# Performance work log

Hardware: AMD Instinct MI355X
Metric: run time of the kernel (lower is better)

## Reference

```python
import jax, jax.numpy as jnp
import numpy as np

N_ATOMS = 100000
N_EDGES = 1000000
HIDDEN = 64
OUT_DIM = 128
N_LAYERS = 3
N_ELEMENTS = 100


def setup_inputs() -> dict:
    key = jax.random.key(0)
    ks = jax.random.split(key, 14)
    s = 0.05
    return {
        "atomic_numbers": jax.random.randint(ks[0], (N_ATOMS,), 0, N_ELEMENTS),
        "positions": jax.random.normal(ks[1], (N_ATOMS, 3), jnp.float32),
        "lattice": jax.random.normal(ks[2], (3, 3), jnp.float32),
        "edge_index": jax.random.randint(ks[3], (2, N_EDGES), 0, N_ATOMS),
        "emb_table": jax.random.normal(ks[4], (N_ELEMENTS, HIDDEN), jnp.float32) * s,
        "W_lin": jax.random.normal(ks[5], (N_LAYERS, HIDDEN, HIDDEN), jnp.float32) * s,
        "b_lin": jax.random.normal(ks[6], (N_LAYERS, HIDDEN), jnp.float32) * s,
        "W_gate": jax.random.normal(ks[7], (N_LAYERS, 2 * HIDDEN, HIDDEN), jnp.float32) * s,
        "b_gate": jax.random.normal(ks[8], (N_LAYERS, HIDDEN), jnp.float32) * s,
        "W_out1": jax.random.normal(ks[9], (HIDDEN, HIDDEN), jnp.float32) * s,
        "b_out1": jax.random.normal(ks[10], (HIDDEN,), jnp.float32) * s,
        "W_out2": jax.random.normal(ks[11], (HIDDEN, OUT_DIM), jnp.float32) * s,
        "b_out2": jax.random.normal(ks[12], (OUT_DIM,), jnp.float32) * s,
    }


def reference(atomic_numbers, positions, lattice, edge_index,
              emb_table, W_lin, b_lin, W_gate, b_gate,
              W_out1, b_out1, W_out2, b_out2):
    # positions/lattice unused when edge_index is provided (matches original).
    x = emb_table[atomic_numbers]            # [N, H] embedding lookup
    row, col = edge_index[0], edge_index[1]
    n = x.shape[0]
    for i in range(W_lin.shape[0]):          # fixed small layer count
        xn = x[col]                          # [E, H] neighbor gather
        gate_in = jnp.concatenate([x[row], xn], axis=-1)  # [E, 2H]
        gate = jax.nn.sigmoid(gate_in @ W_gate[i] + b_gate[i])
        messages = gate * (xn @ W_lin[i] + b_lin[i])       # [E, H]
        agg = jax.ops.segment_sum(messages, row, num_segments=n)  # scatter-add
        x = jax.nn.relu(agg + x @ W_lin[i] + b_lin[i])
    pooled = x.mean(axis=0)                  # [H] mean pool over atoms
    h = jax.nn.relu(pooled @ W_out1 + b_out1)
    return h @ W_out2 + b_out2               # [OUT_DIM]
```

## Files before the change

### kernel.cpp

```cpp
#include <hip/hip_runtime.h>
#include <hip/hip_bf16.h>
#include <stdint.h>


#define H 64
#define BSHIFT 7
#define BROWS 128

typedef __attribute__((ext_vector_type(8))) short bf16x8;
typedef __attribute__((ext_vector_type(4))) float f32x4;

__device__ __forceinline__ float sigmoidf_fast(float z) {
  return __builtin_amdgcn_rcpf(1.f + __expf(-z));
}

__device__ __forceinline__ ushort f2bf(float f) {
  uint32_t u = __float_as_uint(f);
  u = (u + 0x7fffu + ((u >> 16) & 1u)) >> 16;
  return (ushort)u;
}
__device__ __forceinline__ uint32_t pack_gl(float gc, float lin) {
  uint32_t ug = __float_as_uint(gc);
  ug = (ug + 0x7fffu + ((ug >> 16) & 1u)) >> 16;
  uint32_t ul = __float_as_uint(lin);
  ul = ((ul + 0x7fffu + ((ul >> 16) & 1u)) >> 16) << 16;
  return ul | ug;
}
__device__ __forceinline__ float unpack_gc(uint32_t p) {
  return __uint_as_float(p << 16);
}
__device__ __forceinline__ float unpack_lin(uint32_t p) {
  return __uint_as_float(p & 0xffff0000u);
}

__global__ __launch_bounds__(256) void bucket_hist_kernel(
    const int* __restrict__ row, int* __restrict__ bcnt, int E, int nbuck) {
  __shared__ int cnt[1024];
  const int tid = threadIdx.x;
  for (int b = tid; b < nbuck; b += 256) cnt[b] = 0;
  __syncthreads();
  for (int e = blockIdx.x * blockDim.x + tid; e < E; e += gridDim.x * blockDim.x)
    atomicAdd(&cnt[row[e] >> BSHIFT], 1);
  __syncthreads();
  for (int b = tid; b < nbuck; b += 256)
    if (cnt[b]) atomicAdd(&bcnt[b], cnt[b]);
}

__global__ __launch_bounds__(1024) void bucket_scan_kernel(
    const int* __restrict__ bcnt, int* __restrict__ bstart,
    int* __restrict__ bcur, int* __restrict__ offs, int nbuck, int N, int E) {
  __shared__ int sh[1024];
  const int tid = threadIdx.x;
  const int mine = (tid < nbuck) ? bcnt[tid] : 0;
  sh[tid] = mine;
  __syncthreads();
  for (int off = 1; off < 1024; off <<= 1) {
    const int v = (tid >= off) ? sh[tid - off] : 0;
    __syncthreads();
    sh[tid] += v;
    __syncthreads();
  }
  if (tid < nbuck) {
    const int ex = sh[tid] - mine;
    bstart[tid] = ex;
    bcur[tid] = ex;
  }
  if (tid == 0) {
    bstart[nbuck] = E;
    offs[N] = E;
  }
}

#define SCHUNK 4096
__global__ __launch_bounds__(256) void bucket_scatter_kernel(
    const int* __restrict__ row, const int* __restrict__ col,
    int* __restrict__ bcur, uint2* __restrict__ ebuf, int E, int nbuck) {
  __shared__ int cnt[1024], base[1024];
  const int tid = threadIdx.x;
  const int start = blockIdx.x * SCHUNK;
  const int end = min(start + SCHUNK, E);
  for (int b = tid; b < nbuck; b += 256) cnt[b] = 0;
  __syncthreads();
  for (int e = start + tid; e < end; e += 256)
    atomicAdd(&cnt[row[e] >> BSHIFT], 1);
  __syncthreads();
  for (int b = tid; b < nbuck; b += 256) {
    if (cnt[b]) base[b] = atomicAdd(&bcur[b], cnt[b]);
    cnt[b] = 0;
  }
  __syncthreads();
  for (int e = start + tid; e < end; e += 256) {
    const int r = row[e];
    const int b = r >> BSHIFT;
    const int pos = base[b] + atomicAdd(&cnt[b], 1);
    ebuf[pos] = make_uint2((uint32_t)r, (uint32_t)col[e]);
  }
}

__global__ __launch_bounds__(256) void csr_build_kernel(
    const uint2* __restrict__ ebuf, const int* __restrict__ bstart,
    int* __restrict__ offs, int* __restrict__ cols, int N) {
  __shared__ int cnt[BROWS], sc[BROWS];
  const int tid = threadIdx.x;
  const int b = blockIdx.x;
  const int bs = bstart[b], be = bstart[b + 1];
  const int rowbase = b << BSHIFT;
  if (tid < BROWS) cnt[tid] = 0;
  __syncthreads();
  for (int e = bs + tid; e < be; e += 256)
    atomicAdd(&cnt[ebuf[e].x & (BROWS - 1)], 1);
  __syncthreads();
  if (tid < BROWS) sc[tid] = cnt[tid];
  __syncthreads();
  for (int off = 1; off < BROWS; off <<= 1) {
    const int v = (tid >= off && tid < BROWS) ? sc[tid - off] : 0;
    __syncthreads();
    if (tid < BROWS) sc[tid] += v;
    __syncthreads();
  }
  if (tid < BROWS) {
    sc[tid] -= cnt[tid];
    cnt[tid] = 0;
    const int r = rowbase + tid;
    if (r < N) offs[r] = bs + sc[tid];
  }
  __syncthreads();
  for (int e = bs + tid; e < be; e += 256) {
    const uint2 u = ebuf[e];
    const int rl = u.x & (BROWS - 1);
    const int pos = sc[rl] + atomicAdd(&cnt[rl], 1);
    cols[bs + pos] = (int)u.y;
  }
}

template <bool FIRST>
__global__ __launch_bounds__(256) void node_mm3_mfma(
    const ushort* __restrict__ x, const int* __restrict__ an,
    const float* __restrict__ emb, const float* __restrict__ Wl,
    const float* __restrict__ bl, const float* __restrict__ Wgr,
    const float* __restrict__ Wgc, const float* __restrict__ bg,
    float* __restrict__ gr, uint32_t* __restrict__ glpk, int N) {
  const int tid = threadIdx.x;
  const int lane = tid & 63, wid = tid >> 6;
  const int l15 = lane & 15, kg = lane >> 4;

  bf16x8 bfrag[3][4][2];
#pragma unroll
  for (int mat = 0; mat < 3; mat++) {
    const float* Wm = (mat == 0) ? Wl : (mat == 1) ? Wgr : Wgc;
#pragma unroll
    for (int nt = 0; nt < 4; nt++) {
#pragma unroll
      for (int ks = 0; ks < 2; ks++) {
        const float* wp = Wm + (size_t)(ks * 32 + kg * 8) * H + nt * 16 + l15;
        bf16x8 bb;
#pragma unroll
        for (int j = 0; j < 8; j++) bb[j] = (short)f2bf(wp[(size_t)j * H]);
        bfrag[mat][nt][ks] = bb;
      }
    }
  }

  const int mbase = blockIdx.x * 64 + wid * 16;
  const int arow = mbase + l15;
  const int arow_c = min(arow, N - 1);

  bf16x8 afrag0, afrag1;
  if (FIRST) {
    const int a = an[arow_c];
    const float* src = emb + (size_t)a * H + kg * 8;
    const float4 u0 = *(const float4*)(src);
    const float4 u1 = *(const float4*)(src + 4);
    const float4 u2 = *(const float4*)(src + 32);
    const float4 u3 = *(const float4*)(src + 36);
    bf16x8 t0, t1;
    t0[0] = (short)f2bf(u0.x); t0[1] = (short)f2bf(u0.y);
    t0[2] = (short)f2bf(u0.z); t0[3] = (short)f2bf(u0.w);
    t0[4] = (short)f2bf(u1.x); t0[5] = (short)f2bf(u1.y);
    t0[6] = (short)f2bf(u1.z); t0[7] = (short)f2bf(u1.w);
    t1[0] = (short)f2bf(u2.x); t1[1] = (short)f2bf(u2.y);
    t1[2] = (short)f2bf(u2.z); t1[3] = (short)f2bf(u2.w);
    t1[4] = (short)f2bf(u3.x); t1[5] = (short)f2bf(u3.y);
    t1[6] = (short)f2bf(u3.z); t1[7] = (short)f2bf(u3.w);
    afrag0 = t0; afrag1 = t1;
  } else {
    const ushort* src = x + (size_t)arow_c * H + kg * 8;
    afrag0 = *(const bf16x8*)(src);
    afrag1 = *(const bf16x8*)(src + 32);
  }

  f32x4 accL[4], accR[4], accC[4];
#pragma unroll
  for (int nt = 0; nt < 4; nt++) {
    const float blv = bl[nt * 16 + l15];
    const float bgv = bg[nt * 16 + l15];
    accL[nt] = (f32x4){blv, blv, blv, blv};
    accR[nt] = (f32x4){0.f, 0.f, 0.f, 0.f};
    accC[nt] = (f32x4){bgv, bgv, bgv, bgv};
  }
#pragma unroll
  for (int nt = 0; nt < 4; nt++) {
    accL[nt] = __builtin_amdgcn_mfma_f32_16x16x32_bf16(afrag0, bfrag[0][nt][0], accL[nt], 0, 0, 0);
    accL[nt] = __builtin_amdgcn_mfma_f32_16x16x32_bf16(afrag1, bfrag[0][nt][1], accL[nt], 0, 0, 0);
    accR[nt] = __builtin_amdgcn_mfma_f32_16x16x32_bf16(afrag0, bfrag[1][nt][0], accR[nt], 0, 0, 0);
    accR[nt] = __builtin_amdgcn_mfma_f32_16x16x32_bf16(afrag1, bfrag[1][nt][1], accR[nt], 0, 0, 0);
    accC[nt] = __builtin_amdgcn_mfma_f32_16x16x32_bf16(afrag0, bfrag[2][nt][0], accC[nt], 0, 0, 0);
    accC[nt] = __builtin_amdgcn_mfma_f32_16x16x32_bf16(afrag1, bfrag[2][nt][1], accC[nt], 0, 0, 0);
  }
#pragma unroll
  for (int nt = 0; nt < 4; nt++) {
#pragma unroll
    for (int r = 0; r < 4; r++) {
      const int atom = mbase + kg * 4 + r;
      if (atom < N) {
        const size_t o = (size_t)atom * H + nt * 16 + l15;
        gr[o] = accR[nt][r];
        glpk[o] = pack_gl(accC[nt][r], accL[nt][r]);
      }
    }
  }
}

__global__ __launch_bounds__(256) void agg_kernel(
    const float* __restrict__ gr, const uint32_t* __restrict__ glpk,
    const int* __restrict__ offs, const int* __restrict__ cols,
    ushort* __restrict__ x, int N) {
  const int lane = threadIdx.x & 63, w = threadIdx.x >> 6;
  for (int i = blockIdx.x * 4 + w; i < N; i += gridDim.x * 4) {
    const int s = offs[i], e = offs[i + 1];
    const float gri = gr[(size_t)i * H + lane];
    float acc = 0.f;
    for (int cb = s; cb < e; cb += 64) {
      const int nchunk = min(64, e - cb);
      const int myc = (lane < nchunk) ? cols[cb + lane] : 0;
      int j = 0;
      for (; j + 3 < nchunk; j += 4) {
        const int c0 = __shfl(myc, j + 0), c1 = __shfl(myc, j + 1);
        const int c2 = __shfl(myc, j + 2), c3 = __shfl(myc, j + 3);
        const uint32_t p0 = glpk[(size_t)c0 * H + lane];
        const uint32_t p1 = glpk[(size_t)c1 * H + lane];
        const uint32_t p2 = glpk[(size_t)c2 * H + lane];
        const uint32_t p3 = glpk[(size_t)c3 * H + lane];
        acc += unpack_lin(p0) * sigmoidf_fast(gri + unpack_gc(p0));
        acc += unpack_lin(p1) * sigmoidf_fast(gri + unpack_gc(p1));
        acc += unpack_lin(p2) * sigmoidf_fast(gri + unpack_gc(p2));
        acc += unpack_lin(p3) * sigmoidf_fast(gri + unpack_gc(p3));
      }
      for (; j < nchunk; j++) {
        const int c0 = __shfl(myc, j);
        const uint32_t p0 = glpk[(size_t)c0 * H + lane];
        acc += unpack_lin(p0) * sigmoidf_fast(gri + unpack_gc(p0));
      }
    }
    const float li = unpack_lin(glpk[(size_t)i * H + lane]);
    x[(size_t)i * H + lane] = f2bf(fmaxf(acc + li, 0.f));
  }
}

__global__ void pool_kernel(const ushort* __restrict__ x,
                            float* __restrict__ pool, int N) {
  __shared__ float ps[4][64];
  const int tid = threadIdx.x, c = tid & 63, wid = tid >> 6;
  float s = 0.f;
  for (int i = blockIdx.x * 4 + wid; i < N; i += gridDim.x * 4)
    s += __uint_as_float(((uint32_t)x[(size_t)i * H + c]) << 16);
  ps[wid][c] = s;
  __syncthreads();
  if (tid < 64) {
    const float t = ps[0][tid] + ps[1][tid] + ps[2][tid] + ps[3][tid];
    atomicAdd(&pool[tid], t);
  }
}

__global__ void mlp_kernel(const float* __restrict__ pool,
                           const float* __restrict__ W1,
                           const float* __restrict__ b1,
                           const float* __restrict__ W2,
                           const float* __restrict__ b2,
                           float* __restrict__ out, float invN) {
  __shared__ float p[64], h[64];
  const int tid = threadIdx.x;
  if (tid < 64) p[tid] = pool[tid] * invN;
  __syncthreads();
  if (tid < 64) {
    float s = b1[tid];
    for (int k = 0; k < 64; k++) s = fmaf(p[k], W1[k * 64 + tid], s);
    h[tid] = fmaxf(s, 0.f);
  }
  __syncthreads();
  float s = b2[tid];
  for (int k = 0; k < 64; k++) s = fmaf(h[k], W2[k * 128 + tid], s);
  out[tid] = s;
}

extern "C" void kernel_launch(void* const* d_in, const int* in_sizes, int n_in,
                              void* d_out, int out_size, void* d_ws,
                              size_t ws_size, hipStream_t stream) {
  const int*   an  = (const int*)d_in[0];
  const int*   ei  = (const int*)d_in[3];
  const float* emb = (const float*)d_in[4];
  const float* Wl  = (const float*)d_in[5];
  const float* bl  = (const float*)d_in[6];
  const float* Wg  = (const float*)d_in[7];
  const float* bg  = (const float*)d_in[8];
  const float* W1  = (const float*)d_in[9];
  const float* b1  = (const float*)d_in[10];
  const float* W2  = (const float*)d_in[11];
  const float* b2  = (const float*)d_in[12];
  float* out = (float*)d_out;

  const int N = in_sizes[0];
  const int E = in_sizes[3] / 2;
  const int* row = ei;
  const int* col = ei + E;
  const int nbuck = (N + BROWS - 1) >> BSHIFT;

  const size_t NH = (size_t)N * H;
  char* ws = (char*)d_ws;
  ushort*   x    = (ushort*)(ws);
  float*    gr   = (float*)(ws + NH * 2);
  uint32_t* glpk = (uint32_t*)(ws + NH * 2 + NH * 4);
  char* p = ws + NH * 2 + NH * 4 + NH * 4;
  int*   offs   = (int*)p;   p += ((size_t)N + 1) * 4;
  int*   cols   = (int*)p;   p += (size_t)E * 4;
  int*   bcnt   = (int*)p;   p += 4096;
  int*   bstart = (int*)p;   p += 4100;
  int*   bcur   = (int*)p;   p += 4096;
  uint2* ebuf   = (uint2*)p; p += (size_t)E * 8;
  float* pool   = (float*)p;

  hipMemsetAsync(bcnt, 0, (size_t)nbuck * 4, stream);
  bucket_hist_kernel<<<1024, 256, 0, stream>>>(row, bcnt, E, nbuck);
  bucket_scan_kernel<<<1, 1024, 0, stream>>>(bcnt, bstart, bcur, offs, nbuck, N, E);
  bucket_scatter_kernel<<<(E + SCHUNK - 1) / SCHUNK, 256, 0, stream>>>(
      row, col, bcur, ebuf, E, nbuck);
  csr_build_kernel<<<nbuck, 256, 0, stream>>>(ebuf, bstart, offs, cols, N);

  const int mmGrid = (N + 63) / 64;
  const int aggGrid = (N + 3) / 4;
  for (int l = 0; l < 3; l++) {
    const float* Wl_l  = Wl + (size_t)l * H * H;
    const float* bl_l  = bl + (size_t)l * H;
    const float* Wgr_l = Wg + (size_t)l * 2 * H * H;
    const float* Wgc_l = Wgr_l + H * H;
    const float* bg_l  = bg + (size_t)l * H;
    if (l == 0)
      node_mm3_mfma<true><<<mmGrid, 256, 0, stream>>>(
          x, an, emb, Wl_l, bl_l, Wgr_l, Wgc_l, bg_l, gr, glpk, N);
    else
      node_mm3_mfma<false><<<mmGrid, 256, 0, stream>>>(
          x, an, emb, Wl_l, bl_l, Wgr_l, Wgc_l, bg_l, gr, glpk, N);
    agg_kernel<<<aggGrid, 256, 0, stream>>>(gr, glpk, offs, cols, x, N);
  }

  hipMemsetAsync(pool, 0, 64 * sizeof(float), stream);
  pool_kernel<<<1024, 256, 0, stream>>>(x, pool, N);
  mlp_kernel<<<1, 128, 0, stream>>>(pool, W1, b1, W2, b2, out, 1.0f / (float)N);
}
```

Baseline: 403.7 us.

## Pre-pack bf16 weight fragments, fold -log2e into gate weights, unroll gather by 8

Adds a prep kernel that converts the layer weights once into bf16 MFMA fragment layout, with the gate weights and gate bias pre-scaled by -log2(e). This lets the aggregation compute the sigmoid with exp2 and no multiply, and removes the per-block strided fp32 loads and conversions in the node matmul. The edge-gather loop is unrolled to 8 loads in flight to expose more memory parallelism. The pool memset is folded into the scan kernel. Scaling before bf16 rounding changes rounding slightly, and the extra prep launch adds a small fixed cost.

```diff
diff --git a/kernel.cpp b/kernel.cpp
--- a/kernel.cpp
+++ b/kernel.cpp
@@ -6,13 +6,10 @@
 #define H 64
 #define BSHIFT 7
 #define BROWS 128
+#define NLOG2E -1.4426950408889634f
 
 typedef __attribute__((ext_vector_type(8))) short bf16x8;
 typedef __attribute__((ext_vector_type(4))) float f32x4;
-
-__device__ __forceinline__ float sigmoidf_fast(float z) {
-  return __builtin_amdgcn_rcpf(1.f + __expf(-z));
-}
 
 __device__ __forceinline__ ushort f2bf(float f) {
   uint32_t u = __float_as_uint(f);
@@ -32,6 +29,36 @@
 __device__ __forceinline__ float unpack_lin(uint32_t p) {
   return __uint_as_float(p & 0xffff0000u);
 }
+__device__ __forceinline__ float sig_from_neglog2(float arg) {
+  return __builtin_amdgcn_rcpf(1.f + exp2f(arg));
+}
+
+__global__ __launch_bounds__(256) void prep_kernel(
+    const float* __restrict__ Wl, const float* __restrict__ Wg,
+    const float* __restrict__ bg, bf16x8* __restrict__ wprep,
+    float* __restrict__ bgs) {
+  const int t = blockIdx.x * 256 + threadIdx.x;
+  if (t < 192) bgs[t] = bg[t] * NLOG2E;
+  if (t >= 4608) return;
+  const int l = t / 1536;
+  const int rem = t - l * 1536;
+  const int mat = rem >> 9;
+  const int rem2 = rem & 511;
+  const int nt = rem2 >> 7;
+  const int ks = (rem2 >> 6) & 1;
+  const int lane = rem2 & 63;
+  const int kg = lane >> 4, l15 = lane & 15;
+  const float* src;
+  float s;
+  if (mat == 0)      { src = Wl + (size_t)l * 4096;        s = 1.f; }
+  else if (mat == 1) { src = Wg + (size_t)l * 8192;        s = NLOG2E; }
+  else               { src = Wg + (size_t)l * 8192 + 4096; s = NLOG2E; }
+  bf16x8 v;
+#pragma unroll
+  for (int j = 0; j < 8; j++)
+    v[j] = (short)f2bf(src[(size_t)(ks * 32 + kg * 8 + j) * 64 + nt * 16 + l15] * s);
+  wprep[t] = v;
+}
 
 __global__ __launch_bounds__(256) void bucket_hist_kernel(
     const int* __restrict__ row, int* __restrict__ bcnt, int E, int nbuck) {
@@ -48,9 +75,11 @@
 
 __global__ __launch_bounds__(1024) void bucket_scan_kernel(
     const int* __restrict__ bcnt, int* __restrict__ bstart,
-    int* __restrict__ bcur, int* __restrict__ offs, int nbuck, int N, int E) {
+    int* __restrict__ bcur, int* __restrict__ offs, float* __restrict__ pool,
+    int nbuck, int N, int E) {
   __shared__ int sh[1024];
   const int tid = threadIdx.x;
+  if (tid < 64) pool[tid] = 0.f;
   const int mine = (tid < nbuck) ? bcnt[tid] : 0;
   sh[tid] = mine;
   __syncthreads();
@@ -136,9 +165,8 @@
 template <bool FIRST>
 __global__ __launch_bounds__(256) void node_mm3_mfma(
     const ushort* __restrict__ x, const int* __restrict__ an,
-    const float* __restrict__ emb, const float* __restrict__ Wl,
-    const float* __restrict__ bl, const float* __restrict__ Wgr,
-    const float* __restrict__ Wgc, const float* __restrict__ bg,
+    const float* __restrict__ emb, const bf16x8* __restrict__ wp,
+    const float* __restrict__ bl, const float* __restrict__ bgs,
     float* __restrict__ gr, uint32_t* __restrict__ glpk, int N) {
   const int tid = threadIdx.x;
   const int lane = tid & 63, wid = tid >> 6;
@@ -146,20 +174,12 @@
 
   bf16x8 bfrag[3][4][2];
 #pragma unroll
-  for (int mat = 0; mat < 3; mat++) {
-    const float* Wm = (mat == 0) ? Wl : (mat == 1) ? Wgr : Wgc;
-#pragma unroll
-    for (int nt = 0; nt < 4; nt++) {
-#pragma unroll
-      for (int ks = 0; ks < 2; ks++) {
-        const float* wp = Wm + (size_t)(ks * 32 + kg * 8) * H + nt * 16 + l15;
-        bf16x8 bb;
-#pragma unroll
-        for (int j = 0; j < 8; j++) bb[j] = (short)f2bf(wp[(size_t)j * H]);
-        bfrag[mat][nt][ks] = bb;
-      }
-    }
-  }
+  for (int mat = 0; mat < 3; mat++)
+#pragma unroll
+    for (int nt = 0; nt < 4; nt++)
+#pragma unroll
+      for (int ks = 0; ks < 2; ks++)
+        bfrag[mat][nt][ks] = wp[(((mat * 4 + nt) * 2 + ks) << 6) + lane];
 
   const int mbase = blockIdx.x * 64 + wid * 16;
   const int arow = mbase + l15;
@@ -193,7 +213,7 @@
 #pragma unroll
   for (int nt = 0; nt < 4; nt++) {
     const float blv = bl[nt * 16 + l15];
-    const float bgv = bg[nt * 16 + l15];
+    const float bgv = bgs[nt * 16 + l15];
     accL[nt] = (f32x4){blv, blv, blv, blv};
     accR[nt] = (f32x4){0.f, 0.f, 0.f, 0.f};
     accC[nt] = (f32x4){bgv, bgv, bgv, bgv};
@@ -234,22 +254,21 @@
       const int nchunk = min(64, e - cb);
       const int myc = (lane < nchunk) ? cols[cb + lane] : 0;
       int j = 0;
-      for (; j + 3 < nchunk; j += 4) {
-        const int c0 = __shfl(myc, j + 0), c1 = __shfl(myc, j + 1);
-        const int c2 = __shfl(myc, j + 2), c3 = __shfl(myc, j + 3);
-        const uint32_t p0 = glpk[(size_t)c0 * H + lane];
-        const uint32_t p1 = glpk[(size_t)c1 * H + lane];
-        const uint32_t p2 = glpk[(size_t)c2 * H + lane];
-        const uint32_t p3 = glpk[(size_t)c3 * H + lane];
-        acc += unpack_lin(p0) * sigmoidf_fast(gri + unpack_gc(p0));
-        acc += unpack_lin(p1) * sigmoidf_fast(gri + unpack_gc(p1));
-        acc += unpack_lin(p2) * sigmoidf_fast(gri + unpack_gc(p2));
-        acc += unpack_lin(p3) * sigmoidf_fast(gri + unpack_gc(p3));
+      for (; j + 7 < nchunk; j += 8) {
+        uint32_t p[8];
+#pragma unroll
+        for (int q = 0; q < 8; q++) {
+          const int c = __shfl(myc, j + q);
+          p[q] = glpk[(size_t)c * H + lane];
+        }
+#pragma unroll
+        for (int q = 0; q < 8; q++)
+          acc += unpack_lin(p[q]) * sig_from_neglog2(gri + unpack_gc(p[q]));
       }
       for (; j < nchunk; j++) {
-        const int c0 = __shfl(myc, j);
-        const uint32_t p0 = glpk[(size_t)c0 * H + lane];
-        acc += unpack_lin(p0) * sigmoidf_fast(gri + unpack_gc(p0));
+        const int c = __shfl(myc, j);
+        const uint32_t p0 = glpk[(size_t)c * H + lane];
+        acc += unpack_lin(p0) * sig_from_neglog2(gri + unpack_gc(p0));
       }
     }
     const float li = unpack_lin(glpk[(size_t)i * H + lane]);
@@ -321,17 +340,22 @@
   float*    gr   = (float*)(ws + NH * 2);
   uint32_t* glpk = (uint32_t*)(ws + NH * 2 + NH * 4);
   char* p = ws + NH * 2 + NH * 4 + NH * 4;
-  int*   offs   = (int*)p;   p += ((size_t)N + 1) * 4;
-  int*   cols   = (int*)p;   p += (size_t)E * 4;
-  int*   bcnt   = (int*)p;   p += 4096;
-  int*   bstart = (int*)p;   p += 4100;
-  int*   bcur   = (int*)p;   p += 4096;
-  uint2* ebuf   = (uint2*)p; p += (size_t)E * 8;
-  float* pool   = (float*)p;
+  int*    offs   = (int*)p;    p += ((size_t)N + 1) * 4;
+  int*    cols   = (int*)p;    p += (size_t)E * 4;
+  int*    bcnt   = (int*)p;    p += 4096;
+  int*    bstart = (int*)p;    p += 4100;
+  int*    bcur   = (int*)p;    p += 4096;
+  uint2*  ebuf   = (uint2*)p;  p += (size_t)E * 8;
+  bf16x8* wprep  = (bf16x8*)p; p += 4608 * 16;
+  float*  bgs    = (float*)p;  p += 192 * 4;
+  float*  pool   = (float*)p;
+
+  prep_kernel<<<18, 256, 0, stream>>>(Wl, Wg, bg, wprep, bgs);
 
   hipMemsetAsync(bcnt, 0, (size_t)nbuck * 4, stream);
   bucket_hist_kernel<<<1024, 256, 0, stream>>>(row, bcnt, E, nbuck);
-  bucket_scan_kernel<<<1, 1024, 0, stream>>>(bcnt, bstart, bcur, offs, nbuck, N, E);
+  bucket_scan_kernel<<<1, 1024, 0, stream>>>(bcnt, bstart, bcur, offs, pool,
+                                             nbuck, N, E);
   bucket_scatter_kernel<<<(E + SCHUNK - 1) / SCHUNK, 256, 0, stream>>>(
       row, col, bcur, ebuf, E, nbuck);
   csr_build_kernel<<<nbuck, 256, 0, stream>>>(ebuf, bstart, offs, cols, N);
@@ -339,21 +363,18 @@
   const int mmGrid = (N + 63) / 64;
   const int aggGrid = (N + 3) / 4;
   for (int l = 0; l < 3; l++) {
-    const float* Wl_l  = Wl + (size_t)l * H * H;
-    const float* bl_l  = bl + (size_t)l * H;
-    const float* Wgr_l = Wg + (size_t)l * 2 * H * H;
-    const float* Wgc_l = Wgr_l + H * H;
-    const float* bg_l  = bg + (size_t)l * H;
+    const bf16x8* wp  = wprep + (size_t)l * 1536;
+    const float*  bll = bl + (size_t)l * H;
+    const float*  bgl = bgs + (size_t)l * H;
     if (l == 0)
-      node_mm3_mfma<true><<<mmGrid, 256, 0, stream>>>(
-          x, an, emb, Wl_l, bl_l, Wgr_l, Wgc_l, bg_l, gr, glpk, N);
+      node_mm3_mfma<true><<<mmGrid, 256, 0, stream>>>(x, an, emb, wp, bll, bgl,
+                                                      gr, glpk, N);
     else
-      node_mm3_mfma<false><<<mmGrid, 256, 0, stream>>>(
-          x, an, emb, Wl_l, bl_l, Wgr_l, Wgc_l, bg_l, gr, glpk, N);
+      node_mm3_mfma<false><<<mmGrid, 256, 0, stream>>>(x, an, emb, wp, bll, bgl,
+                                                       gr, glpk, N);
     agg_kernel<<<aggGrid, 256, 0, stream>>>(gr, glpk, offs, cols, x, N);
   }
 
-  hipMemsetAsync(pool, 0, 64 * sizeof(float), stream);
   pool_kernel<<<1024, 256, 0, stream>>>(x, pool, N);
   mlp_kernel<<<1, 128, 0, stream>>>(pool, W1, b1, W2, b2, out, 1.0f / (float)N);
 }
```

Result: no change. 400.9 us (-0.7%).
